# Optimization experiments

Measured on AMD Instinct MI355X. Metric: run time of the kernel, lower is better.

## Reference

```python
import jax, jax.numpy as jnp
import numpy as np

NUM_GRAPHS = 131072
NUM_NODES = 25


def setup_inputs() -> dict:
    key = jax.random.key(0)
    k1, k2, k3 = jax.random.split(key, 3)
    G, N = NUM_GRAPHS, NUM_NODES
    x = jax.random.normal(k1, (G * N, 1), dtype=jnp.float32)
    # skeleton tree shared across graphs: root has parent -1, parent(i) = (i-1)//2
    p = np.empty(N, dtype=np.int64)
    p[0] = -1
    p[1:] = (np.arange(1, N) - 1) // 2
    parent = jnp.asarray(np.tile(p, G))
    offset = jax.random.normal(k2, (G * N, 6), dtype=jnp.float32)
    ax = jax.random.normal(k3, (N, 3), dtype=jnp.float32)  # per-node axes, shared across graphs
    axis = jnp.tile(ax, (G, 1))
    return {"x": x, "parent": parent, "offset": offset, "num_graphs": G, "axis": axis}


def _single_axis(e, axis_name):
    # e: [G, N] -> [G, N, 3, 3]
    c, s = jnp.cos(e), jnp.sin(e)
    z, o = jnp.zeros_like(c), jnp.ones_like(c)
    if axis_name == 'x':
        rows = [[o, z, z], [z, c, -s], [z, s, c]]
    elif axis_name == 'y':
        rows = [[c, z, s], [z, o, z], [-s, z, c]]
    else:  # 'z'
        rows = [[c, -s, z], [s, c, z], [z, z, o]]
    return jnp.stack([jnp.stack(r, axis=-1) for r in rows], axis=-2)


def _euler_xyz(rpy):
    # order 'xyz': Rz(rpy_z) @ Ry(rpy_y) @ Rx(rpy_x), matching transform_from_euler
    Rz = _single_axis(rpy[..., 2], 'z')
    Ry = _single_axis(rpy[..., 1], 'y')
    Rx = _single_axis(rpy[..., 0], 'x')
    return jnp.einsum('gnij,gnjk,gnkl->gnil', Rz, Ry, Rx)


def _rodrigues(theta, n):
    # theta: [G, N]; n: [N, 3] raw (unnormalized) axis, matching the original module
    c, s = jnp.cos(theta), jnp.sin(theta)
    v = 1.0 - c
    n1, n2, n3 = n[..., 0], n[..., 1], n[..., 2]
    rows = [
        [c + n1 * n1 * v, n1 * n2 * v - n3 * s, n1 * n3 * v + n2 * s],
        [n1 * n2 * v + n3 * s, c + n2 * n2 * v, n2 * n3 * v - n1 * s],
        [n1 * n3 * v - n2 * s, n2 * n3 * v + n1 * s, c + n3 * n3 * v],
    ]
    return jnp.stack([jnp.stack(r, axis=-1) for r in rows], axis=-2)


def _fk(x, offset, axis, parent_np, num_graphs):
    x = x.reshape(num_graphs, -1)          # [G, N]
    G, N = x.shape
    ax = axis.reshape(G, -1, 3)[0]          # [N, 3] (first graph only, like the original)
    theta = x * jnp.linalg.norm(ax, axis=-1)  # angle scaled by axis norm
    off = offset.reshape(G, -1, 6)
    xyz, rpy = off[..., :3], off[..., 3:]
    # per-node local rotation: rpy_transform @ axis_transform, [G, N, 3, 3]
    local = jnp.einsum('gnij,gnjk->gnik', _euler_xyz(rpy), _rodrigues(theta, ax))
    pos = [None] * N
    gpos = [None] * N
    rot = [None] * N
    for i in range(N):  # loop over fixed small skeleton (tree dependency)
        p = int(parent_np[i])
        if p == -1:
            pos[i] = jnp.zeros((G, 3), dtype=x.dtype)
            gpos[i] = xyz[:, i]
            rot[i] = local[:, i]
        else:
            d = jnp.einsum('gij,gj->gi', rot[p], xyz[:, i])
            pos[i] = d + pos[p]
            gpos[i] = d + gpos[p]
            rot[i] = jnp.einsum('gij,gjk->gik', rot[p], local[:, i])
    positions = jnp.stack(pos, axis=1).reshape(-1, 3)
    rot_matrices = jnp.stack(rot, axis=1).reshape(-1, 3, 3)
    global_positions = jnp.stack(gpos, axis=1).reshape(-1, 3)
    return positions, rot_matrices, global_positions


def reference(x, parent, offset, num_graphs, axis):
    parent_np = np.asarray(jax.device_get(parent)).reshape(num_graphs, -1)[0]
    return _fk(x, offset, axis, parent_np, num_graphs)
```

## Files before the change

kernel.cpp:

```cpp
#include <hip/hip_runtime.h>
#include <math.h>

#define NG 131072
#define NN 25
#define BT 128

__device__ __forceinline__ void mat3mul(const float* __restrict__ A,
                                        const float* __restrict__ B,
                                        float* __restrict__ C) {
#pragma unroll
    for (int i = 0; i < 3; ++i) {
#pragma unroll
        for (int j = 0; j < 3; ++j) {
            C[i * 3 + j] = A[i * 3 + 0] * B[0 + j]
                         + A[i * 3 + 1] * B[3 + j]
                         + A[i * 3 + 2] * B[6 + j];
        }
    }
}

__device__ __forceinline__ void local_rot(float roll, float pitch, float yaw,
                                          float theta, float a1, float a2, float a3,
                                          float* __restrict__ M) {
    float sx, cx, sy, cy, sz, cz, s, c;
    __sincosf(roll,  &sx, &cx);
    __sincosf(pitch, &sy, &cy);
    __sincosf(yaw,   &sz, &cz);
    __sincosf(theta, &s,  &c);
    float E[9];
    E[0] = cz * cy; E[1] = cz * sy * sx - sz * cx; E[2] = cz * sy * cx + sz * sx;
    E[3] = sz * cy; E[4] = sz * sy * sx + cz * cx; E[5] = sz * sy * cx - cz * sx;
    E[6] = -sy;     E[7] = cy * sx;                E[8] = cy * cx;
    const float v = 1.0f - c;
    float Q[9];
    Q[0] = c + a1 * a1 * v;  Q[1] = a1 * a2 * v - a3 * s;  Q[2] = a1 * a3 * v + a2 * s;
    Q[3] = a1 * a2 * v + a3 * s;  Q[4] = c + a2 * a2 * v;  Q[5] = a2 * a3 * v - a1 * s;
    Q[6] = a1 * a3 * v - a2 * s;  Q[7] = a2 * a3 * v + a1 * s;  Q[8] = c + a3 * a3 * v;
    mat3mul(E, Q, M);
}

__global__ __launch_bounds__(BT, 1)
void fk_kernel(const float* __restrict__ x,
               const float* __restrict__ offset,
               const float* __restrict__ axis,
               float* __restrict__ out)
{
    __shared__ __align__(16) float lds[15360];

    const int tid = threadIdx.x;
    const long long blk = blockIdx.x;
    const long long g = blk * BT + tid;

    const float* __restrict__ xg   = x + g * NN;
    const float* __restrict__ offg = offset + g * NN * 6;

    float* __restrict__ out_pos  = out;
    float* __restrict__ out_rot  = out + (long long)NG * NN * 3;
    float* __restrict__ out_gpos = out + (long long)NG * NN * 12;

    float R[13][9];
    float rx = 0.f, ry = 0.f, rz = 0.f;

    float* lpos  = lds;
    float* lroot = lds + BT * 75;

#pragma unroll
    for (int n = 0; n < NN; ++n) {
        const int p = (n - 1) >> 1;
        float2 o01 = *(const float2*)(offg + n * 6);
        float  tz  = offg[n * 6 + 2];

        float px, py, pz;
        if (n == 0) {
            rx = o01.x; ry = o01.y; rz = tz;
            px = 0.f; py = 0.f; pz = 0.f;
        } else {
            const float* pr = R[p];
            const float ppx = lpos[tid * 75 + p * 3 + 0];
            const float ppy = lpos[tid * 75 + p * 3 + 1];
            const float ppz = lpos[tid * 75 + p * 3 + 2];
            px = pr[0] * o01.x + pr[1] * o01.y + pr[2] * tz + ppx;
            py = pr[3] * o01.x + pr[4] * o01.y + pr[5] * tz + ppy;
            pz = pr[6] * o01.x + pr[7] * o01.y + pr[8] * tz + ppz;
        }
        lpos[tid * 75 + n * 3 + 0] = px;
        lpos[tid * 75 + n * 3 + 1] = py;
        lpos[tid * 75 + n * 3 + 2] = pz;

        if (n <= 12) {
            const float roll = offg[n * 6 + 3];
            float2 o45 = *(const float2*)(offg + n * 6 + 4);
            const float a1 = axis[n * 3 + 0];
            const float a2 = axis[n * 3 + 1];
            const float a3 = axis[n * 3 + 2];
            const float L = sqrtf(a1 * a1 + a2 * a2 + a3 * a3);
            const float theta = xg[n] * L;
            float M[9];
            local_rot(roll, o45.x, o45.y, theta, a1, a2, a3, M);
            if (n == 0) {
#pragma unroll
                for (int k = 0; k < 9; ++k) R[0][k] = M[k];
            } else {
                mat3mul(R[p], M, R[n]);
            }
        }
    }
    lroot[tid * 3 + 0] = rx;
    lroot[tid * 3 + 1] = ry;
    lroot[tid * 3 + 2] = rz;
    __syncthreads();

    {
        const float4* lp4 = (const float4*)lds;
        float4* dp = (float4*)(out_pos  + blk * (BT * 75));
        float4* dg = (float4*)(out_gpos + blk * (BT * 75));
        for (int i = tid; i < BT * 75 / 4; i += BT) {
            float4 v = lp4[i];
            dp[i] = v;
            const int b = 4 * i;
            float4 w;
            w.x = v.x + lroot[((b + 0) / 75) * 3 + ((b + 0) % 3)];
            w.y = v.y + lroot[((b + 1) / 75) * 3 + ((b + 1) % 3)];
            w.z = v.z + lroot[((b + 2) / 75) * 3 + ((b + 2) % 3)];
            w.w = v.w + lroot[((b + 3) / 75) * 3 + ((b + 3) % 3)];
            dg[i] = w;
        }
    }
    __syncthreads();

#pragma unroll
    for (int n = 0; n <= 12; ++n) {
#pragma unroll
        for (int k = 0; k < 9; ++k) lds[tid * 117 + n * 9 + k] = R[n][k];
    }
    __syncthreads();
    {
        float* dr = out_rot + blk * (long long)(BT * 225);
        for (int i = tid; i < BT * 117; i += BT) {
            const int g2 = i / 117;
            const int f  = i - g2 * 117;
            dr[g2 * 225 + f] = lds[g2 * 117 + f];
        }
    }
    __syncthreads();

#pragma unroll
    for (int n = 13; n < NN; ++n) {
        const int p = (n - 1) >> 1;
        const float roll = offg[n * 6 + 3];
        float2 o45 = *(const float2*)(offg + n * 6 + 4);
        const float a1 = axis[n * 3 + 0];
        const float a2 = axis[n * 3 + 1];
        const float a3 = axis[n * 3 + 2];
        const float L = sqrtf(a1 * a1 + a2 * a2 + a3 * a3);
        const float theta = xg[n] * L;
        float M[9], Rn[9];
        local_rot(roll, o45.x, o45.y, theta, a1, a2, a3, M);
        mat3mul(R[p], M, Rn);
#pragma unroll
        for (int k = 0; k < 9; ++k) lds[tid * 109 + (n - 13) * 9 + k] = Rn[k];
    }
    __syncthreads();

    {
        float* dr = out_rot + blk * (long long)(BT * 225) + 117;
        for (int i = tid; i < BT * 108; i += BT) {
            const int g2 = i / 108;
            const int f  = i - g2 * 108;
            dr[g2 * 225 + f] = lds[g2 * 109 + f];
        }
    }
}

extern "C" void kernel_launch(void* const* d_in, const int* in_sizes, int n_in,
                              void* d_out, int out_size, void* d_ws, size_t ws_size,
                              hipStream_t stream) {
    const float* x      = (const float*)d_in[0];
    const float* offset = (const float*)d_in[2];
    const float* axis   = (const float*)d_in[4];
    float* out = (float*)d_out;

    fk_kernel<<<dim3(NG / BT), dim3(BT), 0, stream>>>(x, offset, axis, out);
}
```

Baseline: 330.8 us.

## Shrink LDS staging and block size to raise occupancy for FK kernel

Cuts the block to 64 threads and replaces the 60 KB shared buffer with a 78-float-per-thread staging area, so more workgroups fit per CU (launch bounds now request 2). Parent positions are kept in registers instead of being reread from LDS. Rotation output is staged and written in three 75-float chunks, computing the leaf rotations between chunks. Output copies become scalar coalesced stores with incremental index arithmetic instead of float4 stores with divisions. Holding all 25 rotations in registers raises register pressure, which may spill.

```diff
diff --git a/kernel.cpp b/kernel.cpp
--- a/kernel.cpp
+++ b/kernel.cpp
@@ -3,7 +3,7 @@
 
 #define NG 131072
 #define NN 25
-#define BT 128
+#define BT 64
 
 __device__ __forceinline__ void mat3mul(const float* __restrict__ A,
                                         const float* __restrict__ B,
@@ -39,64 +39,75 @@
     mat3mul(E, Q, M);
 }
 
-__global__ __launch_bounds__(BT, 1)
+__device__ __forceinline__ void leaf_rot_node(int n,
+        const float* __restrict__ offg, const float* __restrict__ xg,
+        const float* __restrict__ axis, float (*__restrict__ R)[9]) {
+    const int p = (n - 1) >> 1;
+    const float2 t23 = *(const float2*)(offg + n * 6 + 2);
+    const float2 t45 = *(const float2*)(offg + n * 6 + 4);
+    const float a1 = axis[n * 3 + 0];
+    const float a2 = axis[n * 3 + 1];
+    const float a3 = axis[n * 3 + 2];
+    const float L = sqrtf(a1 * a1 + a2 * a2 + a3 * a3);
+    const float theta = xg[n] * L;
+    float M[9];
+    local_rot(t23.y, t45.x, t45.y, theta, a1, a2, a3, M);
+    mat3mul(R[p], M, R[n]);
+}
+
+__global__ __launch_bounds__(BT, 2)
 void fk_kernel(const float* __restrict__ x,
                const float* __restrict__ offset,
                const float* __restrict__ axis,
                float* __restrict__ out)
 {
-    __shared__ __align__(16) float lds[15360];
+    __shared__ __align__(16) float buf[BT * 78];
 
     const int tid = threadIdx.x;
     const long long blk = blockIdx.x;
     const long long g = blk * BT + tid;
 
     const float* __restrict__ xg   = x + g * NN;
-    const float* __restrict__ offg = offset + g * NN * 6;
+    const float* __restrict__ offg = offset + g * (NN * 6);
 
     float* __restrict__ out_pos  = out;
     float* __restrict__ out_rot  = out + (long long)NG * NN * 3;
     float* __restrict__ out_gpos = out + (long long)NG * NN * 12;
 
-    float R[13][9];
+    float R[NN][9];
+    float pp[12][3];
     float rx = 0.f, ry = 0.f, rz = 0.f;
-
-    float* lpos  = lds;
-    float* lroot = lds + BT * 75;
 
 #pragma unroll
     for (int n = 0; n < NN; ++n) {
         const int p = (n - 1) >> 1;
-        float2 o01 = *(const float2*)(offg + n * 6);
-        float  tz  = offg[n * 6 + 2];
+        const float2 t01 = *(const float2*)(offg + n * 6);
+        const float2 t23 = *(const float2*)(offg + n * 6 + 2);
 
         float px, py, pz;
         if (n == 0) {
-            rx = o01.x; ry = o01.y; rz = tz;
+            rx = t01.x; ry = t01.y; rz = t23.x;
             px = 0.f; py = 0.f; pz = 0.f;
         } else {
             const float* pr = R[p];
-            const float ppx = lpos[tid * 75 + p * 3 + 0];
-            const float ppy = lpos[tid * 75 + p * 3 + 1];
-            const float ppz = lpos[tid * 75 + p * 3 + 2];
-            px = pr[0] * o01.x + pr[1] * o01.y + pr[2] * tz + ppx;
-            py = pr[3] * o01.x + pr[4] * o01.y + pr[5] * tz + ppy;
-            pz = pr[6] * o01.x + pr[7] * o01.y + pr[8] * tz + ppz;
+            px = pr[0] * t01.x + pr[1] * t01.y + pr[2] * t23.x + pp[p][0];
+            py = pr[3] * t01.x + pr[4] * t01.y + pr[5] * t23.x + pp[p][1];
+            pz = pr[6] * t01.x + pr[7] * t01.y + pr[8] * t23.x + pp[p][2];
         }
-        lpos[tid * 75 + n * 3 + 0] = px;
-        lpos[tid * 75 + n * 3 + 1] = py;
-        lpos[tid * 75 + n * 3 + 2] = pz;
+        if (n < 12) { pp[n][0] = px; pp[n][1] = py; pp[n][2] = pz; }
+        buf[tid * 78 + n * 3 + 0] = px;
+        buf[tid * 78 + n * 3 + 1] = py;
+        buf[tid * 78 + n * 3 + 2] = pz;
 
-        if (n <= 12) {
-            const float roll = offg[n * 6 + 3];
-            float2 o45 = *(const float2*)(offg + n * 6 + 4);
+        if (n <= 11) {
+            const float2 t45 = *(const float2*)(offg + n * 6 + 4);
             const float a1 = axis[n * 3 + 0];
             const float a2 = axis[n * 3 + 1];
             const float a3 = axis[n * 3 + 2];
             const float L = sqrtf(a1 * a1 + a2 * a2 + a3 * a3);
             const float theta = xg[n] * L;
             float M[9];
-            local_rot(roll, o45.x, o45.y, theta, a1, a2, a3, M);
+            local_rot(t23.y, t45.x, t45.y, theta, a1, a2, a3, M);
             if (n == 0) {
 #pragma unroll
                 for (int k = 0; k < 9; ++k) R[0][k] = M[k];
@@ -105,69 +116,71 @@
             }
         }
     }
-    lroot[tid * 3 + 0] = rx;
-    lroot[tid * 3 + 1] = ry;
-    lroot[tid * 3 + 2] = rz;
+    buf[tid * 78 + 75] = rx;
+    buf[tid * 78 + 76] = ry;
+    buf[tid * 78 + 77] = rz;
     __syncthreads();
 
     {
-        const float4* lp4 = (const float4*)lds;
-        float4* dp = (float4*)(out_pos  + blk * (BT * 75));
-        float4* dg = (float4*)(out_gpos + blk * (BT * 75));
-        for (int i = tid; i < BT * 75 / 4; i += BT) {
-            float4 v = lp4[i];
+        float* __restrict__ dp = out_pos  + blk * (BT * 75);
+        float* __restrict__ dg = out_gpos + blk * (BT * 75);
+        int q = 0, f = tid, m = tid - (tid / 3) * 3;
+        for (int it = 0; it < 75; ++it) {
+            const float v = buf[q * 78 + f];
+            const float r = buf[q * 78 + 75 + m];
+            const int i = it * BT + tid;
             dp[i] = v;
-            const int b = 4 * i;
-            float4 w;
-            w.x = v.x + lroot[((b + 0) / 75) * 3 + ((b + 0) % 3)];
-            w.y = v.y + lroot[((b + 1) / 75) * 3 + ((b + 1) % 3)];
-            w.z = v.z + lroot[((b + 2) / 75) * 3 + ((b + 2) % 3)];
-            w.w = v.w + lroot[((b + 3) / 75) * 3 + ((b + 3) % 3)];
-            dg[i] = w;
+            dg[i] = v + r;
+            f += BT; if (f >= 75) { f -= 75; ++q; }
+            ++m; if (m == 3) m = 0;
+        }
+    }
+    __syncthreads();
+
+    float* __restrict__ dr = out_rot + blk * (long long)(BT * 225);
+
+#pragma unroll
+    for (int f = 0; f < 75; ++f) buf[tid * 78 + f] = R[f / 9][f % 9];
+    __syncthreads();
+    {
+        int q = 0, f = tid;
+        for (int it = 0; it < 75; ++it) {
+            dr[q * 225 + f] = buf[q * 78 + f];
+            f += BT; if (f >= 75) { f -= 75; ++q; }
         }
     }
     __syncthreads();
 
 #pragma unroll
-    for (int n = 0; n <= 12; ++n) {
+    for (int n = 12; n <= 16; ++n) leaf_rot_node(n, offg, xg, axis, R);
 #pragma unroll
-        for (int k = 0; k < 9; ++k) lds[tid * 117 + n * 9 + k] = R[n][k];
+    for (int f = 0; f < 75; ++f) {
+        const int F = 75 + f;
+        buf[tid * 78 + f] = R[F / 9][F % 9];
     }
     __syncthreads();
     {
-        float* dr = out_rot + blk * (long long)(BT * 225);
-        for (int i = tid; i < BT * 117; i += BT) {
-            const int g2 = i / 117;
-            const int f  = i - g2 * 117;
-            dr[g2 * 225 + f] = lds[g2 * 117 + f];
+        int q = 0, f = tid;
+        for (int it = 0; it < 75; ++it) {
+            dr[q * 225 + 75 + f] = buf[q * 78 + f];
+            f += BT; if (f >= 75) { f -= 75; ++q; }
         }
     }
     __syncthreads();
 
 #pragma unroll
-    for (int n = 13; n < NN; ++n) {
-        const int p = (n - 1) >> 1;
-        const float roll = offg[n * 6 + 3];
-        float2 o45 = *(const float2*)(offg + n * 6 + 4);
-        const float a1 = axis[n * 3 + 0];
-        const float a2 = axis[n * 3 + 1];
-        const float a3 = axis[n * 3 + 2];
-        const float L = sqrtf(a1 * a1 + a2 * a2 + a3 * a3);
-        const float theta = xg[n] * L;
-        float M[9], Rn[9];
-        local_rot(roll, o45.x, o45.y, theta, a1, a2, a3, M);
-        mat3mul(R[p], M, Rn);
+    for (int n = 17; n < NN; ++n) leaf_rot_node(n, offg, xg, axis, R);
 #pragma unroll
-        for (int k = 0; k < 9; ++k) lds[tid * 109 + (n - 13) * 9 + k] = Rn[k];
+    for (int f = 0; f < 75; ++f) {
+        const int F = 150 + f;
+        buf[tid * 78 + f] = R[F / 9][F % 9];
     }
     __syncthreads();
-
     {
-        float* dr = out_rot + blk * (long long)(BT * 225) + 117;
-        for (int i = tid; i < BT * 108; i += BT) {
-            const int g2 = i / 108;
-            const int f  = i - g2 * 108;
-            dr[g2 * 225 + f] = lds[g2 * 109 + f];
+        int q = 0, f = tid;
+        for (int it = 0; it < 75; ++it) {
+            dr[q * 225 + 150 + f] = buf[q * 78 + f];
+            f += BT; if (f >= 75) { f -= 75; ++q; }
         }
     }
 }
```

Measured after the change: 353.8 us. 7.0% more time.
